# Optimization experiments

Measured on AMD Instinct MI355X. Metric: run time of the kernel, lower is better.

The kernel has to match this reference:

```python
import jax, jax.numpy as jnp
import numpy as np

B, H, L, D = 2, 16, 2048, 64


def setup_inputs() -> dict:
    key = jax.random.key(0)
    ks = jax.random.split(key, 5)
    q = jax.random.normal(ks[0], (B, H, L, D), dtype=jnp.float32)
    k = jax.random.normal(ks[1], (B, H, L, D), dtype=jnp.float32)
    v = jax.random.normal(ks[2], (B, H, L, D), dtype=jnp.float32)
    pe_q = jax.random.normal(ks[3], (B, H, L, D), dtype=jnp.float32)
    pe_k = jax.random.normal(ks[4], (B, H, L, D), dtype=jnp.float32)
    # causal mask, broadcast over batch: True = keep
    mask = jnp.broadcast_to(jnp.tril(jnp.ones((L, L), dtype=bool)), (B, L, L))
    return {"q": q, "k": k, "v": v, "pe_q": pe_q, "pe_k": pe_k, "mask": mask}


def reference(q, k, v, pe_q, pe_k, mask):
    scale = q.shape[-1] ** (-0.5)
    # dual-score: content QK^T + positional PE_Q PE_K^T, fused before softmax
    attn = (jnp.einsum('bhqd,bhkd->bhqk', q, k)
            + jnp.einsum('bhqd,bhkd->bhqk', pe_q, pe_k)) * scale
    # mask: [B, L, L] -> [B, 1, L, L]; False positions get -inf
    attn = jnp.where(mask[:, None, :, :], attn, -jnp.inf)
    attn = jax.nn.softmax(attn, axis=-1)
    return jnp.einsum('bhqk,bhkd->bhqd', attn, v)
```

## Files before the change

### kernel.cpp

```cpp
#include <hip/hip_runtime.h>
#include <hip/hip_bf16.h>


typedef unsigned short u16;
typedef unsigned int   u32;
typedef __attribute__((ext_vector_type(8))) short bf16x8;
typedef __attribute__((ext_vector_type(4))) float f32x4;

#define L_SEQ 2048
#define D_DIM 64
#define BQ    64
#define BK    32
#define NQT   (L_SEQ / BQ)

__device__ __forceinline__ float bf2f(u32 lo16) {
    u32 u = lo16 << 16; float f; __builtin_memcpy(&f, &u, 4); return f;
}

__device__ __forceinline__ u32 pack_hi16(u32 lo_src, u32 hi_src) {
    return __builtin_amdgcn_perm(hi_src, lo_src, 0x07060302u);
}

__global__ void detect_dtype_kernel(const u16* __restrict__ q, int* __restrict__ flag) {
    const int lane = threadIdx.x;
    float x = fabsf(bf2f((u32)q[lane]));
    bool big = !(x <= 100.f);
    unsigned long long m = __ballot(big);
    if (lane == 0) *flag = (m != 0ull) ? 1 : 0;
}

__device__ __forceinline__ void split_pack(const float* x, uint4& h, uint4& l) {
    u32 xb[8], rb[8];
#pragma unroll
    for (int j = 0; j < 8; ++j) {
        __builtin_memcpy(&xb[j], &x[j], 4);
        u32 hb = xb[j] & 0xffff0000u;
        float hf; __builtin_memcpy(&hf, &hb, 4);
        float r = x[j] - hf;
        __builtin_memcpy(&rb[j], &r, 4);
    }
    h.x = pack_hi16(xb[0], xb[1]);
    h.y = pack_hi16(xb[2], xb[3]);
    h.z = pack_hi16(xb[4], xb[5]);
    h.w = pack_hi16(xb[6], xb[7]);
    l.x = pack_hi16(rb[0], rb[1]);
    l.y = pack_hi16(rb[2], rb[3]);
    l.z = pack_hi16(rb[4], rb[5]);
    l.w = pack_hi16(rb[6], rb[7]);
}

template<bool IS_F32>
__device__ __forceinline__ void unpack8(const uint4& a, const uint4& b, float* x) {
    if (IS_F32) {
        u32 w[8] = {a.x, a.y, a.z, a.w, b.x, b.y, b.z, b.w};
#pragma unroll
        for (int j = 0; j < 8; ++j) __builtin_memcpy(&x[j], &w[j], 4);
    } else {
        u32 w[4] = {a.x, a.y, a.z, a.w};
#pragma unroll
        for (int j = 0; j < 4; ++j) {
            x[2*j]   = bf2f(w[j] & 0xffffu);
            x[2*j+1] = bf2f(w[j] >> 16);
        }
    }
}

struct StKE { uint4 k0, k1, e0, e1; };
struct StV  { u32 v[8]; };

template<bool IS_F32>
__device__ __forceinline__ void issue_ke(const void* Kv, const void* Ev,
        size_t base, int kbase, int r, int j8, StKE& R) {
    const size_t off = base + (size_t)(kbase + r) * D_DIM + j8 * 8;
    if (IS_F32) {
        const uint4* kp = (const uint4*)((const float*)Kv + off);
        R.k0 = kp[0]; R.k1 = kp[1];
        const uint4* ep = (const uint4*)((const float*)Ev + off);
        R.e0 = ep[0]; R.e1 = ep[1];
    } else {
        R.k0 = *(const uint4*)((const u16*)Kv + off);
        R.e0 = *(const uint4*)((const u16*)Ev + off);
    }
}

template<bool IS_F32>
__device__ __forceinline__ void issue_v(const void* Vv,
        size_t base, int kbase, int d, int kg, StV& R) {
    const size_t off = base + (size_t)(kbase + kg * 8) * D_DIM + d;
    if (IS_F32) {
        const u32* vp = (const u32*)((const float*)Vv + off);
#pragma unroll
        for (int j = 0; j < 8; ++j) R.v[j] = vp[j * D_DIM];
    } else {
        const u16* vp = (const u16*)Vv + off;
#pragma unroll
        for (int j = 0; j < 8; ++j) R.v[j] = (u32)vp[j * D_DIM];
    }
}

#define MFMA(a, b, c) __builtin_amdgcn_mfma_f32_16x16x32_bf16((a), (b), (c), 0, 0, 0)

template<bool IS_F32>
__global__ __launch_bounds__(512, 4) void attn_pair(
    const void* __restrict__ Qv, const void* __restrict__ Kv,
    const void* __restrict__ Vv, const void* __restrict__ PQv,
    const void* __restrict__ PKv, void* __restrict__ Ov,
    const int* __restrict__ flag)
{
    if (((*flag) != 0) != IS_F32) return;

    const int bh   = blockIdx.y;
    int qa = ((int)blockIdx.x + bh) & 15;
    if (bh & 16) qa = 15 - qa;
    const int t    = threadIdx.x;
    const int w    = t >> 6;
    const int lane = t & 63;
    const int g    = lane >> 4;
    const int c    = lane & 15;
    const size_t base = (size_t)bh * L_SEQ * D_DIM;
    const int qtile = (w < 4) ? qa : (31 - qa);
    const int qb_w  = qtile * BQ + (w & 3) * 16;
    const int nkt   = 64 - 2 * qa;

    __shared__ __align__(16) u16 Kt[2][BK * 128];
    __shared__ __align__(16) u16 Et[2][BK * 128];
    __shared__ __align__(16) u16 Vt[2][32 * 128];

    bf16x8 qa_h[4], qa_l[4];
    {
        const int qrow = qb_w + c;
#pragma unroll
        for (int ch = 0; ch < 4; ++ch) {
            const void* src = (ch < 2) ? Qv : PQv;
            const int d0 = (ch & 1) * 32 + 8 * g;
            const size_t off = base + (size_t)qrow * D_DIM + d0;
            float x[8];
            if (IS_F32) {
                const uint4* gp = (const uint4*)((const float*)src + off);
                unpack8<true>(gp[0], gp[1], x);
            } else {
                uint4 a = *(const uint4*)((const u16*)src + off);
                unpack8<false>(a, a, x);
            }
#pragma unroll
            for (int j = 0; j < 8; ++j) x[j] *= 0.1803368801f;
            uint4 hp, lp; split_pack(x, hp, lp);
            u32 hw[4] = {hp.x, hp.y, hp.z, hp.w}, lw[4] = {lp.x, lp.y, lp.z, lp.w};
#pragma unroll
            for (int j = 0; j < 4; ++j) {
                qa_h[ch][2*j]   = (short)(hw[j] & 0xffffu);
                qa_h[ch][2*j+1] = (short)(hw[j] >> 16);
                qa_l[ch][2*j]   = (short)(lw[j] & 0xffffu);
                qa_l[ch][2*j+1] = (short)(lw[j] >> 16);
            }
        }
    }

    float mr = -INFINITY, lr = 0.f;
    f32x4 acc[4];
#pragma unroll
    for (int df = 0; df < 4; ++df) acc[df] = (f32x4){0.f, 0.f, 0.f, 0.f};

    const bool is_ke = (t < 256);
    const int ts   = t & 255;
    const int r_t  = ts >> 3;
    const int j8_t = ts & 7;
    const int d_t  = ts & 63;
    const int kg_t = (ts >> 6) & 3;
    const int ke_wo = r_t * 128 + (j8_t ^ (r_t & 7)) * 8;
    const int v_rr  = d_t >> 1;
    const int v_wo  = v_rr * 128 + ((4 * (d_t & 1) + kg_t) ^ (v_rr & 7)) * 8;

    StKE Rke; StV Rv;

    auto stage_store = [&](int b) {
        if (is_ke) {
            float x[8]; uint4 hp, lp;
            unpack8<IS_F32>(Rke.k0, Rke.k1, x);
            split_pack(x, hp, lp);
            *(uint4*)(&Kt[b][0] + ke_wo)      = hp;
            *(uint4*)(&Kt[b][0] + ke_wo + 64) = lp;
            unpack8<IS_F32>(Rke.e0, Rke.e1, x);
            split_pack(x, hp, lp);
            *(uint4*)(&Et[b][0] + ke_wo)      = hp;
            *(uint4*)(&Et[b][0] + ke_wo + 64) = lp;
        } else {
            float x[8]; uint4 hp, lp;
#pragma unroll
            for (int j = 0; j < 8; ++j) {
                if (IS_F32) __builtin_memcpy(&x[j], &Rv.v[j], 4);
                else        x[j] = bf2f(Rv.v[j]);
            }
            split_pack(x, hp, lp);
            *(uint4*)(&Vt[b][0] + v_wo)      = hp;
            *(uint4*)(&Vt[b][0] + v_wo + 64) = lp;
        }
    };
    auto issue = [&](int kbase) {
        if (is_ke) issue_ke<IS_F32>(Kv, PKv, base, kbase, r_t, j8_t, Rke);
        else       issue_v <IS_F32>(Vv, base, kbase, d_t, kg_t, Rv);
    };

    issue(0);
    stage_store(0);
    issue(BK);
    __syncthreads();

    const int c7 = c & 7;
    const int srcA = 32 * (g & 1) + c;
    const int srcB = srcA + 16;
    const int sv = ((4 * (c & 1) + g) ^ ((c >> 1) & 7)) * 8;

    for (int kt = 0; kt < nkt; ++kt) {
        const int cur = kt & 1;
        const int kbase = kt * BK;
        const bool active = (kbase <= qb_w + 15);
        const bool do1 = (kbase + 16 <= qb_w + 15);

        f32x4 s0 = {0,0,0,0}, s1 = {0,0,0,0};
        if (active) {
            const u16* Ktc = &Kt[cur][0];
            const u16* Etc = &Et[cur][0];
            __builtin_amdgcn_s_setprio(1);
#pragma unroll
            for (int ch = 0; ch < 4; ++ch) {
                const u16* Bp = (ch < 2) ? Ktc : Etc;
                const int sh = ((((ch & 1) * 4 + g) ^ c7)) * 8;
                const u16* r0 = Bp + c * 128;
                bf16x8 b0h = *(const bf16x8*)(r0 + sh);
                bf16x8 b0l = *(const bf16x8*)(r0 + sh + 64);
                s0 = MFMA(b0h, qa_h[ch], s0);
                s0 = MFMA(b0l, qa_h[ch], s0);
                s0 = MFMA(b0h, qa_l[ch], s0);
                if (do1) {
                    const u16* r1 = Bp + (c + 16) * 128;
                    bf16x8 b1h = *(const bf16x8*)(r1 + sh);
                    bf16x8 b1l = *(const bf16x8*)(r1 + sh + 64);
                    s1 = MFMA(b1h, qa_h[ch], s1);
                    s1 = MFMA(b1l, qa_h[ch], s1);
                    s1 = MFMA(b1h, qa_l[ch], s1);
                }
            }
            __builtin_amdgcn_s_setprio(0);
        }

        if (kt + 1 < nkt) {
            stage_store(cur ^ 1);
            if (kt + 2 < nkt) issue(kbase + 2 * BK);
        }

        if (active) {
            const u16* Vtc = &Vt[cur][0];
            const int qrow = qb_w + c;
#pragma unroll
            for (int i = 0; i < 4; ++i) {
                if (kbase + 4 * g + i > qrow)                s0[i] = -INFINITY;
                if (!do1 || kbase + 16 + 4 * g + i > qrow)   s1[i] = -INFINITY;
            }
            float vm = fmaxf(fmaxf(fmaxf(s0[0], s0[1]), fmaxf(s0[2], s0[3])),
                             fmaxf(fmaxf(s1[0], s1[1]), fmaxf(s1[2], s1[3])));
            vm = fmaxf(vm, __shfl_xor(vm, 16));
            vm = fmaxf(vm, __shfl_xor(vm, 32));
            float p0f[4], p1f[4];
#pragma unroll
            for (int i = 0; i < 4; ++i) {
                p0f[i] = exp2f(s0[i] - mr);
                p1f[i] = exp2f(s1[i] - mr);
            }
            if (!__all(vm <= mr + 8.f)) {
                const float mn = fmaxf(mr, vm);
                const float al = exp2f(mr - mn);
                mr = mn;
                lr *= al;
                float al4[4];
#pragma unroll
                for (int i = 0; i < 4; ++i) al4[i] = __shfl(al, 20 * g + i);
#pragma unroll
                for (int df = 0; df < 4; ++df) {
#pragma unroll
                    for (int i = 0; i < 4; ++i) acc[df][i] *= al4[i];
                }
#pragma unroll
                for (int i = 0; i < 4; ++i) {
                    p0f[i] = exp2f(s0[i] - mr);
                    p1f[i] = exp2f(s1[i] - mr);
                }
            }
            float rs = (p0f[0] + p0f[1]) + (p0f[2] + p0f[3])
                     + (p1f[0] + p1f[1]) + (p1f[2] + p1f[3]);
            rs += __shfl_xor(rs, 16);
            rs += __shfl_xor(rs, 32);
            lr += rs;
            u32 w0[4], w1[4];
#pragma unroll
            for (int i = 0; i < 4; ++i) {
                const float x0 = p0f[i];
                u32 b0; __builtin_memcpy(&b0, &x0, 4);
                u32 h0 = b0 & 0xffff0000u; float h0f; __builtin_memcpy(&h0f, &h0, 4);
                float l0f = x0 - h0f; u32 l0; __builtin_memcpy(&l0, &l0f, 4);
                w0[i] = pack_hi16(b0, l0);
                const float x1 = p1f[i];
                u32 b1; __builtin_memcpy(&b1, &x1, 4);
                u32 h1 = b1 & 0xffff0000u; float h1f; __builtin_memcpy(&h1f, &h1, 4);
                float l1f = x1 - h1f; u32 l1; __builtin_memcpy(&l1, &l1f, 4);
                w1[i] = pack_hi16(b1, l1);
            }
            const bool lowhalf = (lane < 32);
            bf16x8 pa_h, pa_l;
#pragma unroll
            for (int i = 0; i < 4; ++i) {
                u32 t0a = (u32)__shfl((int)w0[i], srcA);
                u32 t1a = (u32)__shfl((int)w1[i], srcA);
                u32 t0b = (u32)__shfl((int)w0[i], srcB);
                u32 t1b = (u32)__shfl((int)w1[i], srcB);
                u32 ha = lowhalf ? t0a : t1a;
                u32 hb = lowhalf ? t0b : t1b;
                pa_h[i]     = (short)(ha & 0xffffu);
                pa_h[4 + i] = (short)(hb & 0xffffu);
                pa_l[i]     = (short)(ha >> 16);
                pa_l[4 + i] = (short)(hb >> 16);
            }
            __builtin_amdgcn_s_setprio(1);
#pragma unroll
            for (int df = 0; df < 4; ++df) {
                const u16* vw = Vtc + (8 * df + (c >> 1)) * 128;
                bf16x8 vbh = *(const bf16x8*)(vw + sv);
                bf16x8 vbl = *(const bf16x8*)(vw + sv + 64);
                acc[df] = MFMA(pa_h, vbh, acc[df]);
                acc[df] = MFMA(pa_h, vbl, acc[df]);
                acc[df] = MFMA(pa_l, vbh, acc[df]);
            }
            __builtin_amdgcn_s_setprio(0);
        }
        __syncthreads();
    }

    float inv[4];
#pragma unroll
    for (int i = 0; i < 4; ++i) inv[i] = 1.f / __shfl(lr, 20 * g + i);
    if (IS_F32) {
        float* o = (float*)Ov + base;
#pragma unroll
        for (int df = 0; df < 4; ++df)
#pragma unroll
            for (int i = 0; i < 4; ++i)
                o[(size_t)(qb_w + 4 * g + i) * D_DIM + 16 * df + c] = acc[df][i] * inv[i];
    } else {
        __hip_bfloat16* o = (__hip_bfloat16*)Ov + base;
#pragma unroll
        for (int df = 0; df < 4; ++df)
#pragma unroll
            for (int i = 0; i < 4; ++i)
                o[(size_t)(qb_w + 4 * g + i) * D_DIM + 16 * df + c] =
                    __float2bfloat16(acc[df][i] * inv[i]);
    }
}

extern "C" void kernel_launch(void* const* d_in, const int* in_sizes, int n_in,
                              void* d_out, int out_size, void* d_ws, size_t ws_size,
                              hipStream_t stream) {
    const void* q  = d_in[0];
    const void* k  = d_in[1];
    const void* v  = d_in[2];
    const void* pq = d_in[3];
    const void* pk = d_in[4];
    int* flag = (int*)d_ws;

    detect_dtype_kernel<<<1, 64, 0, stream>>>((const u16*)q, flag);

    dim3 grid(NQT / 2, 32);
    attn_pair<false><<<grid, 512, 0, stream>>>(q, k, v, pq, pk, d_out, flag);
    attn_pair<true ><<<grid, 512, 0, stream>>>(q, k, v, pq, pk, d_out, flag);
}
```

Before: 255.8 us.

## Split causal attention key range across blocks and merge partial softmax results

Each block now processes two q-tile segments, each over half of their causal key range, writing unnormalized fp32 partial outputs plus row max and sum to workspace. A separate merge kernel combines the two halves with log-sum-exp rescaling. This balances per-block work, replacing the old tile pairing whose per-block length varied widely. In exchange it adds a large workspace round-trip, an extra kernel launch, and repeated Q loads, and it falls back to the old kernel if the workspace is too small.

```diff
diff --git a/kernel.cpp b/kernel.cpp
--- a/kernel.cpp
+++ b/kernel.cpp
@@ -101,65 +101,27 @@
 #define MFMA(a, b, c) __builtin_amdgcn_mfma_f32_16x16x32_bf16((a), (b), (c), 0, 0, 0)
 
 template<bool IS_F32>
-__global__ __launch_bounds__(512, 4) void attn_pair(
+__global__ __launch_bounds__(512, 4) void attn_split(
     const void* __restrict__ Qv, const void* __restrict__ Kv,
     const void* __restrict__ Vv, const void* __restrict__ PQv,
-    const void* __restrict__ PKv, void* __restrict__ Ov,
-    const int* __restrict__ flag)
+    const void* __restrict__ PKv, float* __restrict__ O_ws,
+    float* __restrict__ ml_ws, const int* __restrict__ flag)
 {
     if (((*flag) != 0) != IS_F32) return;
 
-    const int bh   = blockIdx.y;
-    int qa = ((int)blockIdx.x + bh) & 15;
-    if (bh & 16) qa = 15 - qa;
+    const int bh = blockIdx.y;
+    const int q  = (int)blockIdx.x >> 1;
+    const int h  = (int)blockIdx.x & 1;
     const int t    = threadIdx.x;
     const int w    = t >> 6;
     const int lane = t & 63;
     const int g    = lane >> 4;
     const int c    = lane & 15;
     const size_t base = (size_t)bh * L_SEQ * D_DIM;
-    const int qtile = (w < 4) ? qa : (31 - qa);
-    const int qb_w  = qtile * BQ + (w & 3) * 16;
-    const int nkt   = 64 - 2 * qa;
 
     __shared__ __align__(16) u16 Kt[2][BK * 128];
     __shared__ __align__(16) u16 Et[2][BK * 128];
     __shared__ __align__(16) u16 Vt[2][32 * 128];
-
-    bf16x8 qa_h[4], qa_l[4];
-    {
-        const int qrow = qb_w + c;
-#pragma unroll
-        for (int ch = 0; ch < 4; ++ch) {
-            const void* src = (ch < 2) ? Qv : PQv;
-            const int d0 = (ch & 1) * 32 + 8 * g;
-            const size_t off = base + (size_t)qrow * D_DIM + d0;
-            float x[8];
-            if (IS_F32) {
-                const uint4* gp = (const uint4*)((const float*)src + off);
-                unpack8<true>(gp[0], gp[1], x);
-            } else {
-                uint4 a = *(const uint4*)((const u16*)src + off);
-                unpack8<false>(a, a, x);
-            }
-#pragma unroll
-            for (int j = 0; j < 8; ++j) x[j] *= 0.1803368801f;
-            uint4 hp, lp; split_pack(x, hp, lp);
-            u32 hw[4] = {hp.x, hp.y, hp.z, hp.w}, lw[4] = {lp.x, lp.y, lp.z, lp.w};
-#pragma unroll
-            for (int j = 0; j < 4; ++j) {
-                qa_h[ch][2*j]   = (short)(hw[j] & 0xffffu);
-                qa_h[ch][2*j+1] = (short)(hw[j] >> 16);
-                qa_l[ch][2*j]   = (short)(lw[j] & 0xffffu);
-                qa_l[ch][2*j+1] = (short)(lw[j] >> 16);
-            }
-        }
-    }
-
-    float mr = -INFINITY, lr = 0.f;
-    f32x4 acc[4];
-#pragma unroll
-    for (int df = 0; df < 4; ++df) acc[df] = (f32x4){0.f, 0.f, 0.f, 0.f};
 
     const bool is_ke = (t < 256);
     const int ts   = t & 255;
@@ -196,19 +158,326 @@
             *(uint4*)(&Vt[b][0] + v_wo + 64) = lp;
         }
     };
-    auto issue = [&](int kbase) {
-        if (is_ke) issue_ke<IS_F32>(Kv, PKv, base, kbase, r_t, j8_t, Rke);
-        else       issue_v <IS_F32>(Vv, base, kbase, d_t, kg_t, Rv);
+    auto issue = [&](int kb) {
+        if (is_ke) issue_ke<IS_F32>(Kv, PKv, base, kb, r_t, j8_t, Rke);
+        else       issue_v <IS_F32>(Vv, base, kb, d_t, kg_t, Rv);
     };
-
-    issue(0);
-    stage_store(0);
-    issue(BK);
-    __syncthreads();
 
     const int c7 = c & 7;
     const int srcA = 32 * (g & 1) + c;
     const int srcB = srcA + 16;
+    const int sv = ((4 * (c & 1) + g) ^ ((c >> 1) & 7)) * 8;
+
+    for (int seg = 0; seg < 2; ++seg) {
+        const int s    = seg ? (15 - q) : q;
+        const int half = 2 * s + 2;
+        const int k0   = h ? half : 0;
+        const int klim = k0 + half;
+        const int qtile = 2 * s + ((w >= 4) ? 1 : 0);
+        const int qb_w  = qtile * BQ + (w & 3) * 16;
+
+        bf16x8 qa_h[4], qa_l[4];
+        {
+            const int qrow = qb_w + c;
+#pragma unroll
+            for (int ch = 0; ch < 4; ++ch) {
+                const void* src = (ch < 2) ? Qv : PQv;
+                const int d0 = (ch & 1) * 32 + 8 * g;
+                const size_t off = base + (size_t)qrow * D_DIM + d0;
+                float x[8];
+                if (IS_F32) {
+                    const uint4* gp = (const uint4*)((const float*)src + off);
+                    unpack8<true>(gp[0], gp[1], x);
+                } else {
+                    uint4 a = *(const uint4*)((const u16*)src + off);
+                    unpack8<false>(a, a, x);
+                }
+#pragma unroll
+                for (int j = 0; j < 8; ++j) x[j] *= 0.1803368801f;
+                uint4 hp, lp; split_pack(x, hp, lp);
+                u32 hw[4] = {hp.x, hp.y, hp.z, hp.w}, lw[4] = {lp.x, lp.y, lp.z, lp.w};
+#pragma unroll
+                for (int j = 0; j < 4; ++j) {
+                    qa_h[ch][2*j]   = (short)(hw[j] & 0xffffu);
+                    qa_h[ch][2*j+1] = (short)(hw[j] >> 16);
+                    qa_l[ch][2*j]   = (short)(lw[j] & 0xffffu);
+                    qa_l[ch][2*j+1] = (short)(lw[j] >> 16);
+                }
+            }
+        }
+
+        float mr = -INFINITY, lr = 0.f;
+        f32x4 acc[4];
+#pragma unroll
+        for (int df = 0; df < 4; ++df) acc[df] = (f32x4){0.f, 0.f, 0.f, 0.f};
+
+        issue(k0 * BK);
+        stage_store(0);
+        issue((k0 + 1) * BK);
+        __syncthreads();
+
+        for (int kt = k0; kt < klim; ++kt) {
+            const int cur = (kt - k0) & 1;
+            const int kbase = kt * BK;
+            const bool active = (kbase <= qb_w + 15);
+            const bool do1 = (kbase + 16 <= qb_w + 15);
+
+            f32x4 s0 = {0,0,0,0}, s1 = {0,0,0,0};
+            if (active) {
+                const u16* Ktc = &Kt[cur][0];
+                const u16* Etc = &Et[cur][0];
+                __builtin_amdgcn_s_setprio(1);
+#pragma unroll
+                for (int ch = 0; ch < 4; ++ch) {
+                    const u16* Bp = (ch < 2) ? Ktc : Etc;
+                    const int sh = ((((ch & 1) * 4 + g) ^ c7)) * 8;
+                    const u16* r0 = Bp + c * 128;
+                    bf16x8 b0h = *(const bf16x8*)(r0 + sh);
+                    bf16x8 b0l = *(const bf16x8*)(r0 + sh + 64);
+                    s0 = MFMA(b0h, qa_h[ch], s0);
+                    s0 = MFMA(b0l, qa_h[ch], s0);
+                    s0 = MFMA(b0h, qa_l[ch], s0);
+                    if (do1) {
+                        const u16* r1 = Bp + (c + 16) * 128;
+                        bf16x8 b1h = *(const bf16x8*)(r1 + sh);
+                        bf16x8 b1l = *(const bf16x8*)(r1 + sh + 64);
+                        s1 = MFMA(b1h, qa_h[ch], s1);
+                        s1 = MFMA(b1l, qa_h[ch], s1);
+                        s1 = MFMA(b1h, qa_l[ch], s1);
+                    }
+                }
+                __builtin_amdgcn_s_setprio(0);
+            }
+
+            if (kt + 1 < klim) {
+                stage_store(cur ^ 1);
+                if (kt + 2 < klim) issue((kt + 2) * BK);
+            }
+
+            if (active) {
+                const u16* Vtc = &Vt[cur][0];
+                const int qrow = qb_w + c;
+#pragma unroll
+                for (int i = 0; i < 4; ++i) {
+                    if (kbase + 4 * g + i > qrow)                s0[i] = -INFINITY;
+                    if (!do1 || kbase + 16 + 4 * g + i > qrow)   s1[i] = -INFINITY;
+                }
+                float vm = fmaxf(fmaxf(fmaxf(s0[0], s0[1]), fmaxf(s0[2], s0[3])),
+                                 fmaxf(fmaxf(s1[0], s1[1]), fmaxf(s1[2], s1[3])));
+                vm = fmaxf(vm, __shfl_xor(vm, 16));
+                vm = fmaxf(vm, __shfl_xor(vm, 32));
+                float p0f[4], p1f[4];
+#pragma unroll
+                for (int i = 0; i < 4; ++i) {
+                    p0f[i] = exp2f(s0[i] - mr);
+                    p1f[i] = exp2f(s1[i] - mr);
+                }
+                if (!__all(vm <= mr + 8.f)) {
+                    const float mn = fmaxf(fmaxf(mr, vm), -1.0e30f);
+                    const float al = exp2f(mr - mn);
+                    mr = mn;
+                    lr *= al;
+                    float al4[4];
+#pragma unroll
+                    for (int i = 0; i < 4; ++i) al4[i] = __shfl(al, 20 * g + i);
+#pragma unroll
+                    for (int df = 0; df < 4; ++df) {
+#pragma unroll
+                        for (int i = 0; i < 4; ++i) acc[df][i] *= al4[i];
+                    }
+#pragma unroll
+                    for (int i = 0; i < 4; ++i) {
+                        p0f[i] = exp2f(s0[i] - mr);
+                        p1f[i] = exp2f(s1[i] - mr);
+                    }
+                }
+                float rs = (p0f[0] + p0f[1]) + (p0f[2] + p0f[3])
+                         + (p1f[0] + p1f[1]) + (p1f[2] + p1f[3]);
+                rs += __shfl_xor(rs, 16);
+                rs += __shfl_xor(rs, 32);
+                lr += rs;
+                u32 w0[4], w1[4];
+#pragma unroll
+                for (int i = 0; i < 4; ++i) {
+                    const float x0 = p0f[i];
+                    u32 b0; __builtin_memcpy(&b0, &x0, 4);
+                    u32 h0 = b0 & 0xffff0000u; float h0f; __builtin_memcpy(&h0f, &h0, 4);
+                    float l0f = x0 - h0f; u32 l0; __builtin_memcpy(&l0, &l0f, 4);
+                    w0[i] = pack_hi16(b0, l0);
+                    const float x1 = p1f[i];
+                    u32 b1; __builtin_memcpy(&b1, &x1, 4);
+                    u32 h1 = b1 & 0xffff0000u; float h1f; __builtin_memcpy(&h1f, &h1, 4);
+                    float l1f = x1 - h1f; u32 l1; __builtin_memcpy(&l1, &l1f, 4);
+                    w1[i] = pack_hi16(b1, l1);
+                }
+                const bool lowhalf = (lane < 32);
+                bf16x8 pa_h, pa_l;
+#pragma unroll
+                for (int i = 0; i < 4; ++i) {
+                    u32 t0a = (u32)__shfl((int)w0[i], srcA);
+                    u32 t1a = (u32)__shfl((int)w1[i], srcA);
+                    u32 t0b = (u32)__shfl((int)w0[i], srcB);
+                    u32 t1b = (u32)__shfl((int)w1[i], srcB);
+                    u32 ha = lowhalf ? t0a : t1a;
+                    u32 hb = lowhalf ? t0b : t1b;
+                    pa_h[i]     = (short)(ha & 0xffffu);
+                    pa_h[4 + i] = (short)(hb & 0xffffu);
+                    pa_l[i]     = (short)(ha >> 16);
+                    pa_l[4 + i] = (short)(hb >> 16);
+                }
+                __builtin_amdgcn_s_setprio(1);
+#pragma unroll
+                for (int df = 0; df < 4; ++df) {
+                    const u16* vw = Vtc + (8 * df + (c >> 1)) * 128;
+                    bf16x8 vbh = *(const bf16x8*)(vw + sv);
+                    bf16x8 vbl = *(const bf16x8*)(vw + sv + 64);
+                    acc[df] = MFMA(pa_h, vbh, acc[df]);
+                    acc[df] = MFMA(pa_h, vbl, acc[df]);
+                    acc[df] = MFMA(pa_l, vbh, acc[df]);
+                }
+                __builtin_amdgcn_s_setprio(0);
+            }
+            __syncthreads();
+        }
+
+        const size_t pb = (size_t)h * 32 + bh;
+        float* Op  = O_ws  + pb * (size_t)L_SEQ * D_DIM;
+        float* mlp = ml_ws + pb * (size_t)L_SEQ * 2;
+#pragma unroll
+        for (int df = 0; df < 4; ++df)
+#pragma unroll
+            for (int i = 0; i < 4; ++i)
+                Op[(size_t)(qb_w + 4 * g + i) * D_DIM + 16 * df + c] = acc[df][i];
+        float mrow = __shfl(mr, 20 * g + (c & 3));
+        float lrow = __shfl(lr, 20 * g + (c & 3));
+        if (c < 4) {
+            mlp[(size_t)(qb_w + 4 * g + c) * 2]     = mrow;
+            mlp[(size_t)(qb_w + 4 * g + c) * 2 + 1] = lrow;
+        }
+    }
+}
+
+template<bool IS_F32>
+__global__ __launch_bounds__(64) void merge_kernel(
+    const float* __restrict__ O_ws, const float* __restrict__ ml_ws,
+    void* __restrict__ Ov, const int* __restrict__ flag)
+{
+    if (((*flag) != 0) != IS_F32) return;
+    const int row = blockIdx.x;
+    const int bh  = blockIdx.y;
+    const int d   = threadIdx.x;
+    const size_t idx = (size_t)bh * L_SEQ + row;
+    const size_t hstride_ml = (size_t)32 * L_SEQ * 2;
+    const size_t hstride_o  = (size_t)32 * L_SEQ * D_DIM;
+    const float m0 = ml_ws[idx * 2],              l0 = ml_ws[idx * 2 + 1];
+    const float m1 = ml_ws[hstride_ml + idx * 2], l1 = ml_ws[hstride_ml + idx * 2 + 1];
+    const float m  = fmaxf(m0, m1);
+    const float w0 = exp2f(m0 - m);
+    const float w1 = exp2f(m1 - m);
+    const float l  = l0 * w0 + l1 * w1;
+    const float o  = (O_ws[idx * D_DIM + d] * w0
+                    + O_ws[hstride_o + idx * D_DIM + d] * w1) / l;
+    if (IS_F32) ((float*)Ov)[idx * D_DIM + d] = o;
+    else ((__hip_bfloat16*)Ov)[idx * D_DIM + d] = __float2bfloat16(o);
+}
+
+template<bool IS_F32>
+__global__ __launch_bounds__(512, 4) void attn_fb(
+    const void* __restrict__ Qv, const void* __restrict__ Kv,
+    const void* __restrict__ Vv, const void* __restrict__ PQv,
+    const void* __restrict__ PKv, void* __restrict__ Ov,
+    const int* __restrict__ flag)
+{
+    if (((*flag) != 0) != IS_F32) return;
+    const int bh = blockIdx.y;
+    int qa = ((int)blockIdx.x + bh) & 15;
+    if (bh & 16) qa = 15 - qa;
+    const int t = threadIdx.x, w = t >> 6, lane = t & 63, g = lane >> 4, c = lane & 15;
+    const size_t base = (size_t)bh * L_SEQ * D_DIM;
+    const int qtile = (w < 4) ? qa : (31 - qa);
+    const int qb_w  = qtile * BQ + (w & 3) * 16;
+    const int nkt   = 64 - 2 * qa;
+
+    __shared__ __align__(16) u16 Kt[2][BK * 128];
+    __shared__ __align__(16) u16 Et[2][BK * 128];
+    __shared__ __align__(16) u16 Vt[2][32 * 128];
+
+    bf16x8 qa_h[4], qa_l[4];
+    {
+        const int qrow = qb_w + c;
+#pragma unroll
+        for (int ch = 0; ch < 4; ++ch) {
+            const void* src = (ch < 2) ? Qv : PQv;
+            const int d0 = (ch & 1) * 32 + 8 * g;
+            const size_t off = base + (size_t)qrow * D_DIM + d0;
+            float x[8];
+            if (IS_F32) {
+                const uint4* gp = (const uint4*)((const float*)src + off);
+                unpack8<true>(gp[0], gp[1], x);
+            } else {
+                uint4 a = *(const uint4*)((const u16*)src + off);
+                unpack8<false>(a, a, x);
+            }
+#pragma unroll
+            for (int j = 0; j < 8; ++j) x[j] *= 0.1803368801f;
+            uint4 hp, lp; split_pack(x, hp, lp);
+            u32 hw[4] = {hp.x, hp.y, hp.z, hp.w}, lw[4] = {lp.x, lp.y, lp.z, lp.w};
+#pragma unroll
+            for (int j = 0; j < 4; ++j) {
+                qa_h[ch][2*j]   = (short)(hw[j] & 0xffffu);
+                qa_h[ch][2*j+1] = (short)(hw[j] >> 16);
+                qa_l[ch][2*j]   = (short)(lw[j] & 0xffffu);
+                qa_l[ch][2*j+1] = (short)(lw[j] >> 16);
+            }
+        }
+    }
+
+    float mr = -INFINITY, lr = 0.f;
+    f32x4 acc[4];
+#pragma unroll
+    for (int df = 0; df < 4; ++df) acc[df] = (f32x4){0.f, 0.f, 0.f, 0.f};
+
+    const bool is_ke = (t < 256);
+    const int ts = t & 255;
+    const int r_t = ts >> 3, j8_t = ts & 7, d_t = ts & 63, kg_t = (ts >> 6) & 3;
+    const int ke_wo = r_t * 128 + (j8_t ^ (r_t & 7)) * 8;
+    const int v_rr = d_t >> 1;
+    const int v_wo = v_rr * 128 + ((4 * (d_t & 1) + kg_t) ^ (v_rr & 7)) * 8;
+
+    StKE Rke; StV Rv;
+    auto stage_store = [&](int b) {
+        if (is_ke) {
+            float x[8]; uint4 hp, lp;
+            unpack8<IS_F32>(Rke.k0, Rke.k1, x);
+            split_pack(x, hp, lp);
+            *(uint4*)(&Kt[b][0] + ke_wo) = hp;
+            *(uint4*)(&Kt[b][0] + ke_wo + 64) = lp;
+            unpack8<IS_F32>(Rke.e0, Rke.e1, x);
+            split_pack(x, hp, lp);
+            *(uint4*)(&Et[b][0] + ke_wo) = hp;
+            *(uint4*)(&Et[b][0] + ke_wo + 64) = lp;
+        } else {
+            float x[8]; uint4 hp, lp;
+#pragma unroll
+            for (int j = 0; j < 8; ++j) {
+                if (IS_F32) __builtin_memcpy(&x[j], &Rv.v[j], 4);
+                else        x[j] = bf2f(Rv.v[j]);
+            }
+            split_pack(x, hp, lp);
+            *(uint4*)(&Vt[b][0] + v_wo) = hp;
+            *(uint4*)(&Vt[b][0] + v_wo + 64) = lp;
+        }
+    };
+    auto issue = [&](int kb) {
+        if (is_ke) issue_ke<IS_F32>(Kv, PKv, base, kb, r_t, j8_t, Rke);
+        else       issue_v <IS_F32>(Vv, base, kb, d_t, kg_t, Rv);
+    };
+
+    issue(0); stage_store(0); issue(BK);
+    __syncthreads();
+
+    const int c7 = c & 7;
+    const int srcA = 32 * (g & 1) + c, srcB = srcA + 16;
     const int sv = ((4 * (c & 1) + g) ^ ((c >> 1) & 7)) * 8;
 
     for (int kt = 0; kt < nkt; ++kt) {
@@ -216,7 +485,6 @@
         const int kbase = kt * BK;
         const bool active = (kbase <= qb_w + 15);
         const bool do1 = (kbase + 16 <= qb_w + 15);
-
         f32x4 s0 = {0,0,0,0}, s1 = {0,0,0,0};
         if (active) {
             const u16* Ktc = &Kt[cur][0];
@@ -243,19 +511,17 @@
             }
             __builtin_amdgcn_s_setprio(0);
         }
-
         if (kt + 1 < nkt) {
             stage_store(cur ^ 1);
-            if (kt + 2 < nkt) issue(kbase + 2 * BK);
-        }
-
+            if (kt + 2 < nkt) issue((kt + 2) * BK);
+        }
         if (active) {
             const u16* Vtc = &Vt[cur][0];
             const int qrow = qb_w + c;
 #pragma unroll
             for (int i = 0; i < 4; ++i) {
-                if (kbase + 4 * g + i > qrow)                s0[i] = -INFINITY;
-                if (!do1 || kbase + 16 + 4 * g + i > qrow)   s1[i] = -INFINITY;
+                if (kbase + 4 * g + i > qrow)              s0[i] = -INFINITY;
+                if (!do1 || kbase + 16 + 4 * g + i > qrow) s1[i] = -INFINITY;
             }
             float vm = fmaxf(fmaxf(fmaxf(s0[0], s0[1]), fmaxf(s0[2], s0[3])),
                              fmaxf(fmaxf(s1[0], s1[1]), fmaxf(s1[2], s1[3])));
@@ -368,7 +634,22 @@
 
     detect_dtype_kernel<<<1, 64, 0, stream>>>((const u16*)q, flag);
 
-    dim3 grid(NQT / 2, 32);
-    attn_pair<false><<<grid, 512, 0, stream>>>(q, k, v, pq, pk, d_out, flag);
-    attn_pair<true ><<<grid, 512, 0, stream>>>(q, k, v, pq, pk, d_out, flag);
-}
+    const size_t O_BYTES  = (size_t)2 * 32 * L_SEQ * D_DIM * 4;
+    const size_t ML_BYTES = (size_t)2 * 32 * L_SEQ * 2 * 4;
+    const size_t WS_NEEDED = 256 + O_BYTES + ML_BYTES;
+
+    if (ws_size >= WS_NEEDED) {
+        float* O_ws  = (float*)((char*)d_ws + 256);
+        float* ml_ws = (float*)((char*)d_ws + 256 + O_BYTES);
+        dim3 ag(16, 32);
+        attn_split<false><<<ag, 512, 0, stream>>>(q, k, v, pq, pk, O_ws, ml_ws, flag);
+        attn_split<true ><<<ag, 512, 0, stream>>>(q, k, v, pq, pk, O_ws, ml_ws, flag);
+        dim3 mg(L_SEQ, 32);
+        merge_kernel<false><<<mg, 64, 0, stream>>>(O_ws, ml_ws, d_out, flag);
+        merge_kernel<true ><<<mg, 64, 0, stream>>>(O_ws, ml_ws, d_out, flag);
+    } else {
+        dim3 grid(NQT / 2, 32);
+        attn_fb<false><<<grid, 512, 0, stream>>>(q, k, v, pq, pk, d_out, flag);
+        attn_fb<true ><<<grid, 512, 0, stream>>>(q, k, v, pq, pk, d_out, flag);
+    }
+}
```

Result: slower. 269.2 us (+5.2%).
